# Optimization experiments

Measured on AMD Instinct MI355X. Metric: run time of the kernel, lower is better.

## Reference

```python
import jax, jax.numpy as jnp
import numpy as np

ATTN_BLOCK_SIZE = 4096
NUM_BUCKETS = 64
BUCKET_SIZE = 64
PAST_STEPS = 8
BUCKETS_MINIMUM = 2


def _make_buffers():
    S, B = ATTN_BLOCK_SIZE, NUM_BUCKETS
    idx = np.arange(S)
    arange1 = np.repeat(idx[:, None], S, axis=1)            # [S, S]
    arange2 = ((arange1 - idx[None, :]) % S) // B            # floor-div, nonneg values
    cols = np.arange(B) * B
    arange2 = arange2[:, cols].astype(np.int64)              # [S, B]
    mask = np.tril(np.ones((S, S), dtype=np.float32), k=-BUCKET_SIZE)[:, cols]  # [S, B]
    mask[: BUCKETS_MINIMUM * BUCKET_SIZE] = 0.0
    return arange2, mask


def setup_inputs() -> dict:
    key = jax.random.key(0)
    k1, k2, k3 = jax.random.split(key, 3)
    S, B = ATTN_BLOCK_SIZE, NUM_BUCKETS
    arange2, mask = _make_buffers()
    return {
        "x": jax.random.normal(k1, (16, 16, S, B), dtype=jnp.float32),
        "pb_fwd": jax.random.normal(k2, (1, B), dtype=jnp.float32) * 0.02,
        "pb_bwd": jax.random.normal(k3, (1, B), dtype=jnp.float32) * 0.02,
        "alpha": jnp.ones((1,), dtype=jnp.float32),
        "beta": jnp.full((1,), 0.9, dtype=jnp.float32),
        "arange2": jnp.asarray(arange2),
        "mask": jnp.asarray(mask),
    }


def reference(x, pb_fwd, pb_bwd, alpha, beta, arange2, mask):
    # Training-path forward of Attn_Pred_Model.
    # x: [batch, heads, S, B]; decayed shift-sum over the S (row) axis.
    S = x.shape[-2]
    pad_cfg_tail = [(0, 0)] * (x.ndim - 2)
    result = jnp.zeros_like(x)
    for i in range(PAST_STEPS):  # small fixed unroll, matches torch loop
        shifted = jnp.pad(x[..., : S - (i + 1), :],
                          pad_cfg_tail + [(i + 1, 0), (0, 0)])
        result = result + alpha * (beta ** i) * shifted
    bias_f = pb_fwd[0]                # [B], broadcasts over rows (ones_vec @ param)
    bias_b = pb_bwd[0][arange2]       # gather -> [S, B]
    return (result + bias_f + bias_b) * mask
```

## Files before the change

### kernel.cpp

```cpp
#include <hip/hip_runtime.h>


#define S_DIM 4096
#define B_DIM 64
#define PAST_STEPS 8

__global__ __launch_bounds__(256) void attn_pred_kernel(
    const float* __restrict__ x,
    const float* __restrict__ pb_fwd,
    const float* __restrict__ pb_bwd,
    const float* __restrict__ alpha_p,
    const float* __restrict__ beta_p,
    const float* __restrict__ mask,
    float* __restrict__ out)
{
    const float alpha = alpha_p[0];
    const float beta  = beta_p[0];

    const int tid = blockIdx.x * blockDim.x + threadIdx.x;
    const int j4 = tid & 15;
    const int s  = (tid >> 4) & (S_DIM - 1);
    const int bh = tid >> 16;

    const float4* xp = (const float4*)(x + (size_t)bh * S_DIM * B_DIM);

    float4 acc = make_float4(0.f, 0.f, 0.f, 0.f);
    float coef = alpha;
    #pragma unroll
    for (int i = 0; i < PAST_STEPS; ++i) {
        const int sp = s - 1 - i;
        if (sp >= 0) {
            const float4 v = xp[sp * 16 + j4];
            acc.x += coef * v.x;
            acc.y += coef * v.y;
            acc.z += coef * v.z;
            acc.w += coef * v.w;
        }
        coef *= beta;
    }

    const float4 bf = ((const float4*)pb_fwd)[j4];

    const int base = s - 256 * j4;
    float4 bb;
    bb.x = pb_bwd[((base      ) & (S_DIM - 1)) >> 6];
    bb.y = pb_bwd[((base -  64) & (S_DIM - 1)) >> 6];
    bb.z = pb_bwd[((base - 128) & (S_DIM - 1)) >> 6];
    bb.w = pb_bwd[((base - 192) & (S_DIM - 1)) >> 6];

    const float4 m = ((const float4*)mask)[s * 16 + j4];

    float4 o;
    o.x = (acc.x + bf.x + bb.x) * m.x;
    o.y = (acc.y + bf.y + bb.y) * m.y;
    o.z = (acc.z + bf.z + bb.z) * m.z;
    o.w = (acc.w + bf.w + bb.w) * m.w;

    float4* op = (float4*)(out + (size_t)bh * S_DIM * B_DIM);
    op[s * 16 + j4] = o;
}

extern "C" void kernel_launch(void* const* d_in, const int* in_sizes, int n_in,
                              void* d_out, int out_size, void* d_ws, size_t ws_size,
                              hipStream_t stream) {
    const float* x       = (const float*)d_in[0];
    const float* pb_fwd  = (const float*)d_in[1];
    const float* pb_bwd  = (const float*)d_in[2];
    const float* alpha_p = (const float*)d_in[3];
    const float* beta_p  = (const float*)d_in[4];
    const float* mask    = (const float*)d_in[6];
    float* out = (float*)d_out;

    const int total_f4 = (16 * 16 * S_DIM * B_DIM) / 4;
    dim3 block(256);
    dim3 grid(total_f4 / 256);
    attn_pred_kernel<<<grid, block, 0, stream>>>(x, pb_fwd, pb_bwd, alpha_p,
                                                 beta_p, mask, out);
}
```

Measured before the change: 537.0 us.

## Compute mask analytically, skip masked regions, and reuse rows via sliding window

Each thread now processes a 32-row strip of one float4 column, keeping the last 8 rows of x in registers so each input row is loaded once. The mask buffer is no longer read; the causal/minimum-bucket mask is derived from row and column indices, and fully masked strips just write zeros without touching x. Outputs use nontemporal stores. This relies on the mask having its fixed tril structure and reduces parallelism per element.

```diff
diff --git a/kernel.cpp b/kernel.cpp
--- a/kernel.cpp
+++ b/kernel.cpp
@@ -2,8 +2,13 @@
 
 
 #define S_DIM 4096
-#define B_DIM 64
-#define PAST_STEPS 8
+#define PAST 8
+#define RROWS 32
+#define STRIPS 16
+#define BLOCK_ROWS (RROWS * STRIPS)
+#define BLOCKS_PER_PLANE (S_DIM / BLOCK_ROWS)
+
+typedef float v4f __attribute__((ext_vector_type(4)));
 
 __global__ __launch_bounds__(256) void attn_pred_kernel(
     const float* __restrict__ x,
@@ -11,53 +16,69 @@
     const float* __restrict__ pb_bwd,
     const float* __restrict__ alpha_p,
     const float* __restrict__ beta_p,
-    const float* __restrict__ mask,
     float* __restrict__ out)
 {
+    const int j4 = threadIdx.x & 15;
+    const int st = threadIdx.x >> 4;
+    const int bh = blockIdx.x >> 3;
+    const int s0 = (blockIdx.x & 7) * BLOCK_ROWS + st * RROWS;
+    const int q  = s0 >> 6;
+    const int jb = j4 << 2;
+
+    const size_t plane = (size_t)bh * (S_DIM * 16);
+    const v4f* xp = (const v4f*)x + plane;
+    v4f*       op = (v4f*)out + plane;
+
+    if (s0 < 128 || jb >= q) {
+        const v4f z = (v4f){0.f, 0.f, 0.f, 0.f};
+        #pragma unroll
+        for (int r = 0; r < RROWS; ++r)
+            __builtin_nontemporal_store(z, &op[(s0 + r) * 16 + j4]);
+        return;
+    }
+
     const float alpha = alpha_p[0];
     const float beta  = beta_p[0];
+    float c[PAST];
+    c[0] = alpha;
+    #pragma unroll
+    for (int i = 1; i < PAST; ++i) c[i] = c[i - 1] * beta;
 
-    const int tid = blockIdx.x * blockDim.x + threadIdx.x;
-    const int j4 = tid & 15;
-    const int s  = (tid >> 4) & (S_DIM - 1);
-    const int bh = tid >> 16;
+    const v4f bf = ((const v4f*)pb_fwd)[j4];
+    v4f bias;
+    bias.x = bf.x + pb_bwd[(q - jb    ) & 63];
+    bias.y = bf.y + pb_bwd[(q - jb - 1) & 63];
+    bias.z = bf.z + pb_bwd[(q - jb - 2) & 63];
+    bias.w = bf.w + pb_bwd[(q - jb - 3) & 63];
 
-    const float4* xp = (const float4*)(x + (size_t)bh * S_DIM * B_DIM);
+    v4f mk;
+    mk.x = 1.f;
+    mk.y = (jb + 1 < q) ? 1.f : 0.f;
+    mk.z = (jb + 2 < q) ? 1.f : 0.f;
+    mk.w = (jb + 3 < q) ? 1.f : 0.f;
 
-    float4 acc = make_float4(0.f, 0.f, 0.f, 0.f);
-    float coef = alpha;
+    v4f w[PAST];
     #pragma unroll
-    for (int i = 0; i < PAST_STEPS; ++i) {
-        const int sp = s - 1 - i;
-        if (sp >= 0) {
-            const float4 v = xp[sp * 16 + j4];
-            acc.x += coef * v.x;
-            acc.y += coef * v.y;
-            acc.z += coef * v.z;
-            acc.w += coef * v.w;
+    for (int k = 0; k < PAST; ++k)
+        w[k] = xp[(s0 - PAST + k) * 16 + j4];
+
+    #pragma unroll
+    for (int r = 0; r < RROWS; ++r) {
+        const int s = s0 + r;
+        v4f acc = c[0] * w[PAST - 1];
+        #pragma unroll
+        for (int i = 1; i < PAST; ++i)
+            acc += c[i] * w[PAST - 1 - i];
+        const v4f o = (acc + bias) * mk;
+        __builtin_nontemporal_store(o, &op[s * 16 + j4]);
+
+        if (r + 1 < RROWS) {
+            const v4f nv = xp[s * 16 + j4];
+            #pragma unroll
+            for (int k = 0; k < PAST - 1; ++k) w[k] = w[k + 1];
+            w[PAST - 1] = nv;
         }
-        coef *= beta;
     }
-
-    const float4 bf = ((const float4*)pb_fwd)[j4];
-
-    const int base = s - 256 * j4;
-    float4 bb;
-    bb.x = pb_bwd[((base      ) & (S_DIM - 1)) >> 6];
-    bb.y = pb_bwd[((base -  64) & (S_DIM - 1)) >> 6];
-    bb.z = pb_bwd[((base - 128) & (S_DIM - 1)) >> 6];
-    bb.w = pb_bwd[((base - 192) & (S_DIM - 1)) >> 6];
-
-    const float4 m = ((const float4*)mask)[s * 16 + j4];
-
-    float4 o;
-    o.x = (acc.x + bf.x + bb.x) * m.x;
-    o.y = (acc.y + bf.y + bb.y) * m.y;
-    o.z = (acc.z + bf.z + bb.z) * m.z;
-    o.w = (acc.w + bf.w + bb.w) * m.w;
-
-    float4* op = (float4*)(out + (size_t)bh * S_DIM * B_DIM);
-    op[s * 16 + j4] = o;
 }
 
 extern "C" void kernel_launch(void* const* d_in, const int* in_sizes, int n_in,
@@ -68,12 +89,9 @@
     const float* pb_bwd  = (const float*)d_in[2];
     const float* alpha_p = (const float*)d_in[3];
     const float* beta_p  = (const float*)d_in[4];
-    const float* mask    = (const float*)d_in[6];
     float* out = (float*)d_out;
 
-    const int total_f4 = (16 * 16 * S_DIM * B_DIM) / 4;
-    dim3 block(256);
-    dim3 grid(total_f4 / 256);
-    attn_pred_kernel<<<grid, block, 0, stream>>>(x, pb_fwd, pb_bwd, alpha_p,
-                                                 beta_p, mask, out);
+    const int grid = 16 * 16 * BLOCKS_PER_PLANE;
+    attn_pred_kernel<<<grid, 256, 0, stream>>>(x, pb_fwd, pb_bwd, alpha_p,
+                                               beta_p, out);
 }
```

After: 500.9 us. 6.7% less time.
